# Optimization experiments

Hardware: AMD Instinct MI355X
Metric: run time of the kernel (lower is better)

The kernel has to match this reference:

```python
import jax, jax.numpy as jnp
import numpy as np

NHEAD = 8  # matches init_kwargs

M_NODES = 20000
D_MODEL = 512
N_EDGES = 640000


def setup_inputs() -> dict:
    key = jax.random.key(0)
    ks = jax.random.split(key, 8)
    sc = 1.0 / np.sqrt(D_MODEL)
    return {
        "s": jax.random.normal(ks[0], (M_NODES, D_MODEL), dtype=jnp.float32),
        "edge_index": jax.random.randint(ks[1], (2, N_EDGES), 0, M_NODES, dtype=jnp.int64),
        "Wq": jax.random.normal(ks[2], (D_MODEL, D_MODEL), dtype=jnp.float32) * sc,
        "bq": jax.random.normal(ks[3], (D_MODEL,), dtype=jnp.float32) * sc,
        "Wkv": jax.random.normal(ks[4], (2 * D_MODEL, D_MODEL), dtype=jnp.float32) * sc,
        "bkv": jax.random.normal(ks[5], (2 * D_MODEL,), dtype=jnp.float32) * sc,
        "Wo": jax.random.normal(ks[6], (D_MODEL, D_MODEL), dtype=jnp.float32) * sc,
        "bo": jax.random.normal(ks[7], (D_MODEL,), dtype=jnp.float32) * sc,
    }


def reference(s, edge_index, Wq, bq, Wkv, bkv, Wo, bo):
    M, C = s.shape
    H = NHEAD
    Dh = C // H
    scale = 1.0 / np.sqrt(Dh).astype(np.float32)

    q = (s @ Wq.T + bq).reshape(M, H, Dh)            # [M,H,Dh]
    kv = (s @ Wkv.T + bkv).reshape(M, H, 2 * Dh)     # [M,H,2Dh]
    k, v = kv[..., :Dh], kv[..., Dh:]

    src, tgt = edge_index[0], edge_index[1]

    # per-edge attention logits [E,H]
    a = jnp.einsum('ehc,ehc->eh', q[tgt], k[src]) * scale

    # segment softmax over edges sharing the same target node
    a_max = jax.ops.segment_max(a, tgt, num_segments=M)        # [M,H]
    ex = jnp.exp(a - a_max[tgt])                               # [E,H]
    denom = jax.ops.segment_sum(ex, tgt, num_segments=M)      # [M,H]
    attn = ex / denom[tgt]                                     # [E,H]

    # weighted message aggregation: scatter-sum over target nodes
    o_msg = attn[..., None] * v[src]                           # [E,H,Dh]
    o = jax.ops.segment_sum(o_msg, tgt, num_segments=M)       # [M,H,Dh]
    o = o.reshape(M, C)
    return o @ Wo.T + bo
```

## Files before the change

kernel.cpp:

```cpp
#include <hip/hip_runtime.h>
#include <cmath>

#define MN 20000
#define DM 512
#define NE 640000
#define CAP 128
#define NT 20
#define TSHIFT 10

typedef short  bf16x8 __attribute__((ext_vector_type(8)));
typedef float  f32x4  __attribute__((ext_vector_type(4)));

__device__ __forceinline__ ushort f2b(float x) {
    unsigned u = __builtin_bit_cast(unsigned, x);
    u += 0x7FFF + ((u >> 16) & 1);
    return (ushort)(u >> 16);
}
__device__ __forceinline__ float b2f(ushort b) {
    return __builtin_bit_cast(float, (unsigned)b << 16);
}

#define NS4   (MN * DM / 4)
#define NWC4  (1536 * 512 / 4)
#define NWO4  (512 * 512 / 4)
#define NB4   (1536 / 4)

__device__ __forceinline__ const float* wc_src_row(int r, const float* Wq, const float* Wkv) {
    if (r < 512) return Wq + ((size_t)r << 9);
    if (r < 1024) { int h = (r - 512) >> 6, j = (r - 512) & 63;  return Wkv + ((size_t)(h * 128 + j) << 9); }
    { int h = (r - 1024) >> 6, j = (r - 1024) & 63; return Wkv + ((size_t)(h * 128 + 64 + j) << 9); }
}

__global__ void conv_all_k(const float* __restrict__ s, const float* __restrict__ Wq,
                           const float* __restrict__ Wkv, const float* __restrict__ Wo,
                           const float* __restrict__ bq, const float* __restrict__ bkv,
                           const int* __restrict__ esrc, const int* __restrict__ etgt,
                           int* __restrict__ counts, int* __restrict__ counts2,
                           ushort* __restrict__ s_b, ushort* __restrict__ Wc_b,
                           ushort* __restrict__ Wo_b, float* __restrict__ bc)
{
    int i = blockIdx.x * blockDim.x + threadIdx.x;
    if (i < NE) {
        int t = etgt[i];
        atomicAdd(&counts[t], 1);
        atomicAdd(&counts2[t * NT + (esrc[i] >> TSHIFT)], 1);
    }
    if (i < NS4) {
        float4 v = ((const float4*)s)[i];
        ushort4 o = { f2b(v.x), f2b(v.y), f2b(v.z), f2b(v.w) };
        ((ushort4*)s_b)[i] = o;
        return;
    }
    i -= NS4;
    if (i < NWC4) {
        int e = i * 4, row = e >> 9, col = e & 511;
        float4 v = *(const float4*)(wc_src_row(row, Wq, Wkv) + col);
        ushort4 o = { f2b(v.x), f2b(v.y), f2b(v.z), f2b(v.w) };
        ((ushort4*)Wc_b)[i] = o;
        return;
    }
    i -= NWC4;
    if (i < NWO4) {
        float4 v = ((const float4*)Wo)[i];
        ushort4 o = { f2b(v.x), f2b(v.y), f2b(v.z), f2b(v.w) };
        ((ushort4*)Wo_b)[i] = o;
        return;
    }
    i -= NWO4;
    if (i < NB4) {
#pragma unroll
        for (int u = 0; u < 4; ++u) {
            int r = i * 4 + u;
            float v;
            if (r < 512) v = bq[r];
            else if (r < 1024) { int h = (r - 512) >> 6, j = (r - 512) & 63;  v = bkv[h * 128 + j]; }
            else               { int h = (r - 1024) >> 6, j = (r - 1024) & 63; v = bkv[h * 128 + 64 + j]; }
            bc[r] = v;
        }
    }
}

__global__ __launch_bounds__(512) void gemm_pipe_k(
    const ushort* __restrict__ Ah, const ushort* __restrict__ Bh,
    const float* __restrict__ bias, ushort* __restrict__ Cout,
    int M, int N, int K, int NCB)
{
    __shared__ ushort lds[2][2 * 16384];
    const int nwg = gridDim.x;
    const int o = blockIdx.x;
    const int q8 = nwg >> 3, r8 = nwg & 7, x = o & 7, sl = o >> 3;
    const int wg = (x < r8 ? x * (q8 + 1) : r8 * (q8 + 1) + (x - r8) * q8) + sl;
    const int row0 = (wg / NCB) * 256, col0 = (wg % NCB) * 256;

    const int tid = threadIdx.x;
    const int wid = tid >> 6, l = tid & 63;
    const int wm = (wid >> 2) * 128, wn = (wid & 3) * 64;
    const int fr = l & 15, g = l >> 4;
    const int fcb = g << 4;

    auto STAGE = [&](int bi, int k0) {
#pragma unroll
        for (int p = 0; p < 4; ++p) {
            const int lb  = p * 8192 + tid * 16;
            const int r   = lb >> 7;
            const int cbs = (lb & 127) ^ ((r & 7) << 4);
            const int ar  = min(row0 + r, M - 1);
            const int br  = col0 + r;
            const size_t aoff = (size_t)ar * K + k0 + (cbs >> 1);
            const size_t boff = (size_t)br * K + k0 + (cbs >> 1);
            __builtin_amdgcn_global_load_lds(
                (const __attribute__((address_space(1))) void*)(Ah + aoff),
                (__attribute__((address_space(3))) void*)&lds[bi][0 * 16384 + (lb >> 1)], 16, 0, 0);
            __builtin_amdgcn_global_load_lds(
                (const __attribute__((address_space(1))) void*)(Bh + boff),
                (__attribute__((address_space(3))) void*)&lds[bi][1 * 16384 + (lb >> 1)], 16, 0, 0);
        }
    };

    f32x4 acc[8][4] = {};
    const int NTILES = K >> 6;

    STAGE(0, 0);
    for (int T = 0; T < NTILES; ++T) {
        const int cur = T & 1;
        if (T + 1 < NTILES) {
            STAGE(cur ^ 1, (T + 1) << 6);
            asm volatile("s_waitcnt vmcnt(8)" ::: "memory");
        } else {
            asm volatile("s_waitcnt vmcnt(0)" ::: "memory");
        }
        __builtin_amdgcn_sched_barrier(0);
        __builtin_amdgcn_s_barrier();
        __builtin_amdgcn_sched_barrier(0);

#pragma unroll
        for (int kk = 0; kk < 2; ++kk) {
            bf16x8 a[8], b[4];
#pragma unroll
            for (int m = 0; m < 8; ++m) {
                const int r  = wm + m * 16 + fr;
                const int cb = (kk * 64 + fcb) ^ ((r & 7) << 4);
                a[m] = *(const bf16x8*)&lds[cur][0 * 16384 + r * 64 + (cb >> 1)];
            }
#pragma unroll
            for (int n = 0; n < 4; ++n) {
                const int r  = wn + n * 16 + fr;
                const int cb = (kk * 64 + fcb) ^ ((r & 7) << 4);
                b[n] = *(const bf16x8*)&lds[cur][1 * 16384 + r * 64 + (cb >> 1)];
            }
#pragma unroll
            for (int m = 0; m < 8; ++m)
#pragma unroll
                for (int n = 0; n < 4; ++n)
                    acc[m][n] = __builtin_amdgcn_mfma_f32_16x16x32_bf16(a[m], b[n], acc[m][n], 0, 0, 0);
        }

        __builtin_amdgcn_sched_barrier(0);
        __builtin_amdgcn_s_barrier();
    }

#pragma unroll
    for (int n = 0; n < 4; ++n) {
        const int cg = col0 + wn + n * 16 + fr;
        const float bv = bias[cg];
#pragma unroll
        for (int m = 0; m < 8; ++m) {
#pragma unroll
            for (int j = 0; j < 4; ++j) {
                const int rg = row0 + wm + m * 16 + g * 4 + j;
                if (rg < M) Cout[(size_t)rg * N + cg] = f2b(acc[m][n][j] + bv);
            }
        }
    }
}

__global__ __launch_bounds__(256) void gemm_mfma128(
    const ushort* __restrict__ Ah, const ushort* __restrict__ Bh,
    const float* __restrict__ bias, float* __restrict__ Cout,
    int M, int N, int K, int NCB)
{
    constexpr int LDSH = 128 * 64;
    __shared__ ushort lds[2 * LDSH];
    const int nwg = gridDim.x;
    const int o = blockIdx.x;
    const int q8 = nwg >> 3, r8 = nwg & 7, x = o & 7, sl = o >> 3;
    const int wg = (x < r8 ? x * (q8 + 1) : r8 * (q8 + 1) + (x - r8) * q8) + sl;
    const int row0 = (wg / NCB) * 128, col0 = (wg % NCB) * 128;

    const int tid = threadIdx.x;
    const int wid = tid >> 6, l = tid & 63;
    const int wm = (wid >> 1) * 64, wn = (wid & 1) * 64;
    const int fr = l & 15, g = l >> 4;
    const int fcb = g << 4;

    f32x4 acc[4][4] = {};

    for (int k0 = 0; k0 < K; k0 += 64) {
        __syncthreads();
#pragma unroll
        for (int p = 0; p < 4; ++p) {
            const int lb  = p * 4096 + tid * 16;
            const int r   = lb >> 7;
            const int cbs = (lb & 127) ^ ((r & 7) << 4);
            const int ar  = min(row0 + r, M - 1);
            const int br  = col0 + r;
            const size_t aoff = (size_t)ar * K + k0 + (cbs >> 1);
            const size_t boff = (size_t)br * K + k0 + (cbs >> 1);
            __builtin_amdgcn_global_load_lds(
                (const __attribute__((address_space(1))) void*)(Ah + aoff),
                (__attribute__((address_space(3))) void*)&lds[0 * LDSH + (lb >> 1)], 16, 0, 0);
            __builtin_amdgcn_global_load_lds(
                (const __attribute__((address_space(1))) void*)(Bh + boff),
                (__attribute__((address_space(3))) void*)&lds[1 * LDSH + (lb >> 1)], 16, 0, 0);
        }
        __syncthreads();

#pragma unroll
        for (int kk = 0; kk < 2; ++kk) {
            bf16x8 a[4], b[4];
#pragma unroll
            for (int m = 0; m < 4; ++m) {
                const int r  = wm + m * 16 + fr;
                const int cb = (kk * 64 + fcb) ^ ((r & 7) << 4);
                a[m] = *(const bf16x8*)&lds[0 * LDSH + r * 64 + (cb >> 1)];
            }
#pragma unroll
            for (int n = 0; n < 4; ++n) {
                const int r  = wn + n * 16 + fr;
                const int cb = (kk * 64 + fcb) ^ ((r & 7) << 4);
                b[n] = *(const bf16x8*)&lds[1 * LDSH + r * 64 + (cb >> 1)];
            }
#pragma unroll
            for (int m = 0; m < 4; ++m)
#pragma unroll
                for (int n = 0; n < 4; ++n)
                    acc[m][n] = __builtin_amdgcn_mfma_f32_16x16x32_bf16(a[m], b[n], acc[m][n], 0, 0, 0);
        }
    }

#pragma unroll
    for (int n = 0; n < 4; ++n) {
        const int cg = col0 + wn + n * 16 + fr;
        const float bv = bias[cg];
#pragma unroll
        for (int m = 0; m < 4; ++m) {
#pragma unroll
            for (int j = 0; j < 4; ++j) {
                const int rg = row0 + wm + m * 16 + g * 4 + j;
                if (rg < M) Cout[(size_t)rg * N + cg] = acc[m][n][j] + bv;
            }
        }
    }
}

__global__ __launch_bounds__(1024) void scan_counts_k(
    const int* __restrict__ counts, int* __restrict__ indptr,
    int* __restrict__ dbase, int M)
{
    __shared__ int part[1024];
    __shared__ int hist[128];
    const int t  = threadIdx.x;
    if (t < 128) hist[t] = 0;
    __syncthreads();
    const int CH = (M + 1023) / 1024;
    const int base = t * CH;
    int sum = 0;
    for (int i = 0; i < CH; ++i) {
        int idx = base + i;
        if (idx < M) {
            int c = counts[idx];
            sum += c;
            atomicAdd(&hist[127 - min(c, 127)], 1);
        }
    }
    part[t] = sum;
    __syncthreads();
    for (int off = 1; off < 1024; off <<= 1) {
        int v = (t >= off) ? part[t - off] : 0;
        __syncthreads();
        part[t] += v;
        __syncthreads();
    }
    int excl = part[t] - sum;
    for (int i = 0; i < CH; ++i) {
        int idx = base + i;
        if (idx < M) { indptr[idx] = excl; excl += counts[idx]; }
    }
    if (t == 1023) indptr[M] = part[1023];
    if (t == 0) {
        int run = 0;
        for (int b = 0; b < 128; ++b) { int v = hist[b]; dbase[b] = run; run += v; }
    }
}

__global__ void tileoff_k(const int* __restrict__ indptr, const int* __restrict__ counts2,
                          int* __restrict__ cursor2, int M)
{
    int n = blockIdx.x * blockDim.x + threadIdx.x;
    if (n >= M) return;
    int run = indptr[n];
#pragma unroll
    for (int j = 0; j < NT; ++j) {
        cursor2[n * NT + j] = run;
        run += counts2[n * NT + j];
    }
}

__global__ void scatter_fused_k(const int* __restrict__ src, const int* __restrict__ tgt,
                                int* __restrict__ cursor2, int* __restrict__ slot_off,
                                const int* __restrict__ counts, const int* __restrict__ dbase,
                                int* __restrict__ dcur, int* __restrict__ perm, int E, int M)
{
    int e = blockIdx.x * blockDim.x + threadIdx.x;
    if (e < E) {
        int t = tgt[e], s = src[e];
        int pos = atomicAdd(&cursor2[t * NT + (s >> TSHIFT)], 1);
        slot_off[pos] = s * 3072;
    }
    if (e < M) {
        int b = 127 - min(counts[e], 127);
        int pos = atomicAdd(&dcur[b], 1);
        perm[dbase[b] + pos] = e;
    }
}

__global__ __launch_bounds__(256, 4) void attn11_k(
    const ushort* __restrict__ qkv, const int* __restrict__ indptr,
    const int* __restrict__ slot_off, const int* __restrict__ perm,
    ushort* __restrict__ obh)
{
    __shared__ int slots[4][CAP];
    const int w = threadIdx.x >> 6;
    const int l = threadIdx.x & 63;
    const int node = perm[blockIdx.x * 4 + w];
    const int beg = indptr[node], end = indptr[node + 1];
    const int d = end - beg;
    const int dc = min(d, CAP);

    for (int i = l; i < dc; i += 64) slots[w][i] = slot_off[beg + i];
    __syncthreads();

    const char* base = (const char*)qkv + (l << 4);

    float qf[8];
    {
        bf16x8 qv = *(const bf16x8*)(base + (size_t)node * 3072);
#pragma unroll
        for (int j = 0; j < 8; ++j) qf[j] = b2f((ushort)qv[j]);
    }

    float acc[8] = {};
    float ssum = 0.f;

    int i = 0;
    for (; i + 8 <= dc; i += 8) {
        const int4 sa = *(const int4*)&slots[w][i];
        const int4 sb = *(const int4*)&slots[w][i + 4];
        const char* bp[8] = { base + sa.x, base + sa.y, base + sa.z, base + sa.w,
                              base + sb.x, base + sb.y, base + sb.z, base + sb.w };
        bf16x8 kk[8], vv[8];
#pragma unroll
        for (int u = 0; u < 8; ++u) {
            kk[u] = *(const bf16x8*)(bp[u] + 1024);
            vv[u] = *(const bf16x8*)(bp[u] + 2048);
        }
        float p[8];
#pragma unroll
        for (int u = 0; u < 8; ++u) {
            float pu = 0.f;
#pragma unroll
            for (int j = 0; j < 8; ++j) pu = fmaf(qf[j], b2f((ushort)kk[u][j]), pu);
            p[u] = pu;
        }
#pragma unroll
        for (int u = 0; u < 8; ++u) p[u] += __shfl_xor(p[u], 1);
#pragma unroll
        for (int u = 0; u < 8; ++u) p[u] += __shfl_xor(p[u], 2);
#pragma unroll
        for (int u = 0; u < 8; ++u) p[u] += __shfl_xor(p[u], 4);
        float wt[8];
#pragma unroll
        for (int u = 0; u < 8; ++u) { wt[u] = __expf(p[u] * 0.125f); ssum += wt[u]; }
#pragma unroll
        for (int u = 0; u < 8; ++u)
#pragma unroll
            for (int j = 0; j < 8; ++j) acc[j] = fmaf(wt[u], b2f((ushort)vv[u][j]), acc[j]);
    }
    for (; i < d; ++i) {
        const int so = (i < CAP) ? slots[w][i] : slot_off[beg + i];
        const char* b0 = base + so;
        bf16x8 k0 = *(const bf16x8*)(b0 + 1024);
        bf16x8 v0 = *(const bf16x8*)(b0 + 2048);
        float p0 = 0.f;
#pragma unroll
        for (int j = 0; j < 8; ++j) p0 = fmaf(qf[j], b2f((ushort)k0[j]), p0);
        p0 += __shfl_xor(p0, 1); p0 += __shfl_xor(p0, 2); p0 += __shfl_xor(p0, 4);
        const float w0 = __expf(p0 * 0.125f);
        ssum += w0;
#pragma unroll
        for (int j = 0; j < 8; ++j) acc[j] = fmaf(w0, b2f((ushort)v0[j]), acc[j]);
    }

    const float inv = (d > 0) ? 1.f / ssum : 0.f;
    ushort4 ph0, ph1;
    ph0.x = f2b(acc[0] * inv); ph0.y = f2b(acc[1] * inv);
    ph0.z = f2b(acc[2] * inv); ph0.w = f2b(acc[3] * inv);
    ph1.x = f2b(acc[4] * inv); ph1.y = f2b(acc[5] * inv);
    ph1.z = f2b(acc[6] * inv); ph1.w = f2b(acc[7] * inv);
    const size_t ob_off = (size_t)node * 512 + (l << 3);
    *(ushort4*)(obh + ob_off)     = ph0;
    *(ushort4*)(obh + ob_off + 4) = ph1;
}

extern "C" void kernel_launch(void* const* d_in, const int* in_sizes, int n_in,
                              void* d_out, int out_size, void* d_ws, size_t ws_size,
                              hipStream_t stream)
{
    const float* s   = (const float*)d_in[0];
    const int*   eix = (const int*)d_in[1];
    const float* Wq  = (const float*)d_in[2];
    const float* bq  = (const float*)d_in[3];
    const float* Wkv = (const float*)d_in[4];
    const float* bkv = (const float*)d_in[5];
    const float* Wo  = (const float*)d_in[6];
    const float* bo  = (const float*)d_in[7];
    float* out = (float*)d_out;

    char* ws = (char*)d_ws;
    auto take = [&](size_t bytes) { char* p = ws; ws += (bytes + 255) & ~(size_t)255; return p; };
    ushort* qkv_b  = (ushort*)take((size_t)MN * 1536 * 2);
    ushort* s_b    = (ushort*)take((size_t)MN * 512 * 2);
    ushort* obh    = (ushort*)take((size_t)MN * 512 * 2);
    ushort* Wc_b   = (ushort*)take((size_t)1536 * 512 * 2);
    ushort* Wo_b   = (ushort*)take((size_t)512 * 512 * 2);
    float*  bc     = (float*)take(1536 * 4);
    int* counts    = (int*)take(((size_t)MN + 128 + (size_t)MN * NT) * 4);
    int* dcur      = counts + MN;
    int* counts2   = dcur + 128;
    int* cursor2   = (int*)take((size_t)MN * NT * 4);
    int* slot_off  = (int*)take((size_t)NE * 4);
    int* indptr    = (int*)take((MN + 4) * 4);
    int* dbase     = (int*)take(128 * 4);
    int* perm      = (int*)take(MN * 4);

    hipMemsetAsync(counts, 0, ((size_t)MN + 128 + (size_t)MN * NT) * 4, stream);

    const int convN = NS4 + NWC4 + NWO4 + NB4;
    conv_all_k<<<(convN + 255) / 256, 256, 0, stream>>>(s, Wq, Wkv, Wo, bq, bkv,
                                                        eix, eix + NE, counts, counts2,
                                                        s_b, Wc_b, Wo_b, bc);

    scan_counts_k<<<1, 1024, 0, stream>>>(counts, indptr, dbase, MN);
    tileoff_k<<<(MN + 255) / 256, 256, 0, stream>>>(indptr, counts2, cursor2, MN);
    scatter_fused_k<<<NE / 256, 256, 0, stream>>>(eix, eix + NE, cursor2, slot_off,
                                                  counts, dbase, dcur, perm, NE, MN);

    const int g1 = ((MN + 255) / 256) * (1536 / 256);
    gemm_pipe_k<<<g1, 512, 0, stream>>>(s_b, Wc_b, bc, qkv_b, MN, 1536, DM, 1536 / 256);

    attn11_k<<<MN / 4, 256, 0, stream>>>(qkv_b, indptr, slot_off, perm, obh);

    const int g2 = ((MN + 127) / 128) * (512 / 128);
    gemm_mfma128<<<g2, 256, 0, stream>>>(obh, Wo_b, bo, out, MN, 512, DM, 512 / 128);
}
```

Baseline: 387.2 us.

## Double-buffer LDS in output-projection GEMM and raise wave priority around MFMAs

The output GEMM now uses two LDS buffers, prefetching the next K tile with global_load_lds while computing on the current one, with a vmcnt wait and barriers replacing the two syncthreads per iteration. Both GEMM kernels wrap the MFMA block in s_setprio(1)/s_setprio(0) so compute waves get issue priority. This aims to hide global-to-LDS latency in the small final GEMM, at the cost of doubling LDS use (64KB), which may lower occupancy.

```diff
diff --git a/kernel.cpp b/kernel.cpp
--- a/kernel.cpp
+++ b/kernel.cpp
@@ -133,6 +133,7 @@
         __builtin_amdgcn_s_barrier();
         __builtin_amdgcn_sched_barrier(0);
 
+        __builtin_amdgcn_s_setprio(1);
 #pragma unroll
         for (int kk = 0; kk < 2; ++kk) {
             bf16x8 a[8], b[4];
@@ -154,6 +155,7 @@
                 for (int n = 0; n < 4; ++n)
                     acc[m][n] = __builtin_amdgcn_mfma_f32_16x16x32_bf16(a[m], b[n], acc[m][n], 0, 0, 0);
         }
+        __builtin_amdgcn_s_setprio(0);
 
         __builtin_amdgcn_sched_barrier(0);
         __builtin_amdgcn_s_barrier();
@@ -174,13 +176,12 @@
     }
 }
 
-__global__ __launch_bounds__(256) void gemm_mfma128(
+__global__ __launch_bounds__(256) void gemm_pipe128_k(
     const ushort* __restrict__ Ah, const ushort* __restrict__ Bh,
     const float* __restrict__ bias, float* __restrict__ Cout,
     int M, int N, int K, int NCB)
 {
-    constexpr int LDSH = 128 * 64;
-    __shared__ ushort lds[2 * LDSH];
+    __shared__ ushort lds[2][2 * 8192];
     const int nwg = gridDim.x;
     const int o = blockIdx.x;
     const int q8 = nwg >> 3, r8 = nwg & 7, x = o & 7, sl = o >> 3;
@@ -193,10 +194,7 @@
     const int fr = l & 15, g = l >> 4;
     const int fcb = g << 4;
 
-    f32x4 acc[4][4] = {};
-
-    for (int k0 = 0; k0 < K; k0 += 64) {
-        __syncthreads();
+    auto STAGE = [&](int bi, int k0) {
 #pragma unroll
         for (int p = 0; p < 4; ++p) {
             const int lb  = p * 4096 + tid * 16;
@@ -208,13 +206,30 @@
             const size_t boff = (size_t)br * K + k0 + (cbs >> 1);
             __builtin_amdgcn_global_load_lds(
                 (const __attribute__((address_space(1))) void*)(Ah + aoff),
-                (__attribute__((address_space(3))) void*)&lds[0 * LDSH + (lb >> 1)], 16, 0, 0);
+                (__attribute__((address_space(3))) void*)&lds[bi][0 * 8192 + (lb >> 1)], 16, 0, 0);
             __builtin_amdgcn_global_load_lds(
                 (const __attribute__((address_space(1))) void*)(Bh + boff),
-                (__attribute__((address_space(3))) void*)&lds[1 * LDSH + (lb >> 1)], 16, 0, 0);
-        }
-        __syncthreads();
-
+                (__attribute__((address_space(3))) void*)&lds[bi][1 * 8192 + (lb >> 1)], 16, 0, 0);
+        }
+    };
+
+    f32x4 acc[4][4] = {};
+    const int NTILES = K >> 6;
+
+    STAGE(0, 0);
+    for (int T = 0; T < NTILES; ++T) {
+        const int cur = T & 1;
+        if (T + 1 < NTILES) {
+            STAGE(cur ^ 1, (T + 1) << 6);
+            asm volatile("s_waitcnt vmcnt(8)" ::: "memory");
+        } else {
+            asm volatile("s_waitcnt vmcnt(0)" ::: "memory");
+        }
+        __builtin_amdgcn_sched_barrier(0);
+        __builtin_amdgcn_s_barrier();
+        __builtin_amdgcn_sched_barrier(0);
+
+        __builtin_amdgcn_s_setprio(1);
 #pragma unroll
         for (int kk = 0; kk < 2; ++kk) {
             bf16x8 a[4], b[4];
@@ -222,13 +237,13 @@
             for (int m = 0; m < 4; ++m) {
                 const int r  = wm + m * 16 + fr;
                 const int cb = (kk * 64 + fcb) ^ ((r & 7) << 4);
-                a[m] = *(const bf16x8*)&lds[0 * LDSH + r * 64 + (cb >> 1)];
+                a[m] = *(const bf16x8*)&lds[cur][0 * 8192 + r * 64 + (cb >> 1)];
             }
 #pragma unroll
             for (int n = 0; n < 4; ++n) {
                 const int r  = wn + n * 16 + fr;
                 const int cb = (kk * 64 + fcb) ^ ((r & 7) << 4);
-                b[n] = *(const bf16x8*)&lds[1 * LDSH + r * 64 + (cb >> 1)];
+                b[n] = *(const bf16x8*)&lds[cur][1 * 8192 + r * 64 + (cb >> 1)];
             }
 #pragma unroll
             for (int m = 0; m < 4; ++m)
@@ -236,6 +251,10 @@
                 for (int n = 0; n < 4; ++n)
                     acc[m][n] = __builtin_amdgcn_mfma_f32_16x16x32_bf16(a[m], b[n], acc[m][n], 0, 0, 0);
         }
+        __builtin_amdgcn_s_setprio(0);
+
+        __builtin_amdgcn_sched_barrier(0);
+        __builtin_amdgcn_s_barrier();
     }
 
 #pragma unroll
@@ -461,5 +480,5 @@
     attn11_k<<<MN / 4, 256, 0, stream>>>(qkv_b, indptr, slot_off, perm, obh);
 
     const int g2 = ((MN + 127) / 128) * (512 / 128);
-    gemm_mfma128<<<g2, 256, 0, stream>>>(obh, Wo_b, bo, out, MN, 512, DM, 512 / 128);
-}
+    gemm_pipe128_k<<<g2, 256, 0, stream>>>(obh, Wo_b, bo, out, MN, 512, DM, 512 / 128);
+}
```

Result: no change. 393.0 us (+1.5%).
